# Performance work log

Measured on AMD Instinct MI355X. Metric: run time of the kernel, lower is better.

The kernel has to match this reference:

```python
import jax, jax.numpy as jnp
import numpy as np

N = 50000      # nodes
E = 800000     # edges (before self-loops)
F_IN = 128     # num_features
HID = 32       # hidden channels per head (conv1)
HEADS = 4      # conv1 heads
C = 40         # classes (conv2 out channels)
OUT_HEADS = 1  # conv2 heads
NEG_SLOPE = 0.2


def setup_inputs() -> dict:
    key = jax.random.key(0)
    ks = jax.random.split(key, 10)
    x = jax.random.normal(ks[0], (N, F_IN), jnp.float32)
    edge_index = jax.random.randint(ks[1], (2, E), 0, N, jnp.int32)
    s1 = 1.0 / np.sqrt(F_IN).astype(np.float32)
    s1h = 1.0 / np.sqrt(HID).astype(np.float32)
    s2 = 1.0 / np.sqrt(HEADS * HID).astype(np.float32)
    s2c = 1.0 / np.sqrt(C).astype(np.float32)
    W1 = jax.random.normal(ks[2], (F_IN, HEADS * HID), jnp.float32) * s1
    att_src1 = jax.random.normal(ks[3], (HEADS, HID), jnp.float32) * s1h
    att_dst1 = jax.random.normal(ks[4], (HEADS, HID), jnp.float32) * s1h
    bias1 = jnp.zeros((HEADS * HID,), jnp.float32)
    W2 = jax.random.normal(ks[5], (HEADS * HID, OUT_HEADS * C), jnp.float32) * s2
    att_src2 = jax.random.normal(ks[6], (OUT_HEADS, C), jnp.float32) * s2c
    att_dst2 = jax.random.normal(ks[7], (OUT_HEADS, C), jnp.float32) * s2c
    bias2 = jnp.zeros((C,), jnp.float32)
    return {"x": x, "edge_index": edge_index,
            "W1": W1, "att_src1": att_src1, "att_dst1": att_dst1, "bias1": bias1,
            "W2": W2, "att_src2": att_src2, "att_dst2": att_dst2, "bias2": bias2}


def gat_layer(h_in, src, dst, W, a_src, a_dst, bias, heads, out_ch, concat):
    """PyG GATConv (v1) in inference mode (no dropout on attention)."""
    n = h_in.shape[0]
    h = (h_in @ W).reshape(n, heads, out_ch)              # [N,H,F]
    e_src = jnp.einsum('nhf,hf->nh', h, a_src)            # [N,H]
    e_dst = jnp.einsum('nhf,hf->nh', h, a_dst)            # [N,H]
    alpha = jax.nn.leaky_relu(e_src[src] + e_dst[dst], NEG_SLOPE)  # [E,H]
    # segment softmax over destination-node neighborhoods
    amax = jax.ops.segment_max(alpha, dst, num_segments=n)
    amax = jnp.where(jnp.isfinite(amax), amax, 0.0)
    ex = jnp.exp(alpha - amax[dst])
    denom = jax.ops.segment_sum(ex, dst, num_segments=n)
    coef = ex / (denom[dst] + 1e-16)                      # [E,H]
    # scatter-aggregate weighted source messages
    out = jax.ops.segment_sum(h[src] * coef[:, :, None], dst, num_segments=n)  # [N,H,F]
    out = out.reshape(n, heads * out_ch) if concat else out.mean(axis=1)
    return out + bias


def reference(x, edge_index, W1, att_src1, att_dst1, bias1, W2, att_src2, att_dst2, bias2):
    n = x.shape[0]
    loop = jnp.arange(n, dtype=edge_index.dtype)          # GATConv adds self-loops
    src = jnp.concatenate([edge_index[0], loop])
    dst = jnp.concatenate([edge_index[1], loop])
    h = jax.nn.elu(gat_layer(x, src, dst, W1, att_src1, att_dst1, bias1, HEADS, HID, True))
    out = gat_layer(h, src, dst, W2, att_src2, att_dst2, bias2, OUT_HEADS, C, False)
    return (jax.nn.log_softmax(out, axis=1), jax.nn.softmax(out, axis=1))
```

## Files before the change

kernel.cpp:

```cpp
#include <hip/hip_runtime.h>
#include <hip/hip_bf16.h>

#define F1   128
#define H1   4
#define C2   40
#define NEG  0.2f
#define DS   96
#define EPB  1600
#define BCAP 5632

typedef __hip_bfloat16 bf16;
typedef float f32x2 __attribute__((ext_vector_type(2)));
typedef short s16x8 __attribute__((ext_vector_type(8)));
typedef float f32x4 __attribute__((ext_vector_type(4)));

__device__ __forceinline__ float ldf(const void* p, size_t i, int isbf) {
    return isbf ? __bfloat162float(((const bf16*)p)[i]) : ((const float*)p)[i];
}
__device__ __forceinline__ float lrelu(float a) { return a > 0.f ? a : NEG * a; }

__device__ __forceinline__ unsigned short f2bfb(float f, float& back) {
    unsigned u = __float_as_uint(f);
    unsigned r = u + 0x7FFFu + ((u >> 16) & 1u);
    unsigned short h = (unsigned short)(r >> 16);
    back = __uint_as_float((unsigned)h << 16);
    return h;
}

__device__ __forceinline__ void up2(unsigned g, float& lo, float& hi) {
    lo = __uint_as_float(g << 16);
    hi = __uint_as_float(g & 0xffff0000u);
}
__device__ __forceinline__ f32x2 up2v(unsigned g) {
    f32x2 r;
    r.x = __uint_as_float(g << 16);
    r.y = __uint_as_float(g & 0xffff0000u);
    return r;
}

__device__ __forceinline__ int excl_scan256(int v, int t, int* wsum) {
    int lane = t & 63, wid = t >> 6;
    int orig = v;
#pragma unroll
    for (int o = 1; o < 64; o <<= 1) {
        int n = __shfl_up(v, o, 64);
        if (lane >= o) v += n;
    }
    if (lane == 63) wsum[wid] = v;
    __syncthreads();
    int add = 0;
    for (int k = 0; k < wid; k++) add += wsum[k];
    return v + add - orig;
}

__global__ void k_prep(const unsigned short* __restrict__ x, const void* __restrict__ W1,
                       int* __restrict__ gbin_cnt, int* __restrict__ flag,
                       unsigned short* __restrict__ w1t_hi,
                       unsigned short* __restrict__ w1t_lo) {
    int t = threadIdx.x;
    __shared__ int sh[256];
    int cnt = 0;
    for (int k = t; k < 8192; k += 256)
        if (((x[k] >> 7) & 0xFF) >= 160) cnt++;
    sh[t] = cnt;
    __syncthreads();
    for (int s = 128; s > 0; s >>= 1) {
        if (t < s) sh[t] += sh[t + s];
        __syncthreads();
    }
    const int isbf = (sh[0] < 100) ? 1 : 0;
    if (blockIdx.x == 0) {
        gbin_cnt[t] = 0;
        if (t == 0) flag[0] = isbf;
    }
    int idx = blockIdx.x * 256 + t;
    int k = idx >> 7, c = idx & 127;
    float v = ldf(W1, idx, isbf);
    float back;
    unsigned short hi = f2bfb(v, back);
    float d2;
    unsigned short lo = f2bfb(v - back, d2);
    w1t_hi[c * 128 + k] = hi;
    w1t_lo[c * 128 + k] = isbf ? (unsigned short)0 : lo;
}

__global__ void __launch_bounds__(256) k_scatA(
        const int* __restrict__ ei, int E, int ET, int nbins,
        int* __restrict__ gbin_cnt, unsigned long long* __restrict__ stg) {
    __shared__ int hist[256], lstart[256], gbase[256], lcnt[256];
    __shared__ int wsum[4];
    __shared__ unsigned long long stgl[EPB];
    int t = threadIdx.x;
    hist[t] = 0; lcnt[t] = 0;
    __syncthreads();
    int e0 = blockIdx.x * EPB;
    int e1 = e0 + EPB; if (e1 > ET) e1 = ET;
    for (int e = e0 + t; e < e1; e += 256) {
        int d = (e < E) ? ei[E + e] : (e - E);
        atomicAdd(&hist[d >> 8], 1);
    }
    __syncthreads();
    if (t < nbins && hist[t] > 0) gbase[t] = atomicAdd(&gbin_cnt[t], hist[t]);
    int ls = excl_scan256(hist[t], t, wsum);
    lstart[t] = ls;
    __syncthreads();
    for (int e = e0 + t; e < e1; e += 256) {
        int s, d;
        if (e < E) { s = ei[e]; d = ei[E + e]; }
        else       { s = e - E; d = e - E; }
        int b = d >> 8;
        int r = atomicAdd(&lcnt[b], 1);
        stgl[lstart[b] + r] = ((unsigned long long)(unsigned)d << 32) | (unsigned)s;
    }
    __syncthreads();
    int cntb = e1 - e0;
    for (int i = t; i < cntb; i += 256) {
        unsigned long long p = stgl[i];
        int d = (int)(p >> 32);
        int b = d >> 8;
        int off = gbase[b] + (i - lstart[b]);
        if (off < BCAP) stg[(size_t)b * BCAP + off] = p;
    }
}

__global__ void __launch_bounds__(256) k_gemm1(
        const void* __restrict__ x, const unsigned short* __restrict__ w1t_hi,
        const unsigned short* __restrict__ w1t_lo,
        const void* __restrict__ as1, const void* __restrict__ ad1,
        const int* __restrict__ flag,
        const unsigned long long* __restrict__ stg, const int* __restrict__ gbin_cnt,
        int nbins, int* __restrict__ csr_s, int* __restrict__ rowstart,
        int* __restrict__ deg,
        bf16* __restrict__ h1b, float* __restrict__ es1, float* __restrict__ ed1,
        int N) {
    if (blockIdx.x < nbins) {
        __shared__ int dhist[256], dstart[256], dcnt[256];
        __shared__ int wsum[4];
        __shared__ int out_s[BCAP];
        int bin = blockIdx.x, tt = threadIdx.x;
        int bcnt = gbin_cnt[bin]; if (bcnt > BCAP) bcnt = BCAP;
        dhist[tt] = 0; dcnt[tt] = 0;
        __syncthreads();
        const unsigned long long* mystg = stg + (size_t)bin * BCAP;
        for (int i = tt; i < bcnt; i += 256)
            atomicAdd(&dhist[(int)(mystg[i] >> 32) & 255], 1);
        __syncthreads();
        int dsx = excl_scan256(dhist[tt], tt, wsum);
        dstart[tt] = dsx;
        __syncthreads();
        for (int i = tt; i < bcnt; i += 256) {
            unsigned long long p = mystg[i];
            int ld = (int)(p >> 32) & 255;
            int r = atomicAdd(&dcnt[ld], 1);
            out_s[dstart[ld] + r] = (int)(p & 0xffffffffu);
        }
        __syncthreads();
        size_t gb = (size_t)bin * BCAP;
        for (int i = tt; i < bcnt; i += 256) csr_s[gb + i] = out_s[i];
        int dd = bin * 256 + tt;
        if (dd < N) { rowstart[dd] = (int)gb + dstart[tt]; deg[dd] = dhist[tt]; }
        return;
    }
    const int isbf = flag[0];
    int t = threadIdx.x, wv = t >> 6, l = t & 63;
    int r0 = (wv & 1) * 16, c0 = (wv >> 1) * 64;
    int lr = l & 15, q = l >> 4;
    int n0 = (blockIdx.x - nbins) * 32;
    int rowa = n0 + r0 + lr; if (rowa >= N) rowa = N - 1;

    const bf16*  xb = (const bf16*)x;
    const float* xf = (const float*)x;
    f32x4 acc[4] = {};

#pragma unroll
    for (int ks = 0; ks < 4; ks++) {
        int kb = ks * 32 + q * 8;
        s16x8 ahi, alo;
        if (isbf) {
            ahi = *(const s16x8*)&xb[(size_t)rowa * 128 + kb];
        } else {
            const float* xr = xf + (size_t)rowa * 128 + kb;
            float4 v0 = *(const float4*)xr;
            float4 v1 = *(const float4*)(xr + 4);
            float vv[8] = {v0.x, v0.y, v0.z, v0.w, v1.x, v1.y, v1.z, v1.w};
#pragma unroll
            for (int j = 0; j < 8; j++) {
                float back;
                unsigned short hb = f2bfb(vv[j], back);
                float d2;
                unsigned short lb = f2bfb(vv[j] - back, d2);
                ahi[j] = (short)hb;
                alo[j] = (short)lb;
            }
        }
#pragma unroll
        for (int f = 0; f < 4; f++) {
            int col = c0 + f * 16 + lr;
            s16x8 bh = *(const s16x8*)&w1t_hi[(size_t)col * 128 + kb];
            acc[f] = __builtin_amdgcn_mfma_f32_16x16x32_bf16(ahi, bh, acc[f], 0, 0, 0);
            if (!isbf) {
                s16x8 bl = *(const s16x8*)&w1t_lo[(size_t)col * 128 + kb];
                acc[f] = __builtin_amdgcn_mfma_f32_16x16x32_bf16(alo, bh, acc[f], 0, 0, 0);
                acc[f] = __builtin_amdgcn_mfma_f32_16x16x32_bf16(ahi, bl, acc[f], 0, 0, 0);
            }
        }
    }

    float asv[4], adv[4];
#pragma unroll
    for (int f = 0; f < 4; f++) {
        asv[f] = ldf(as1, c0 + f * 16 + lr, isbf);
        adv[f] = ldf(ad1, c0 + f * 16 + lr, isbf);
    }
    float ps0[4], ps1[4], pd0[4], pd1[4];
#pragma unroll
    for (int r = 0; r < 4; r++) {
        int rw = n0 + r0 + q * 4 + r;
        ps0[r] = acc[0][r] * asv[0] + acc[1][r] * asv[1];
        ps1[r] = acc[2][r] * asv[2] + acc[3][r] * asv[3];
        pd0[r] = acc[0][r] * adv[0] + acc[1][r] * adv[1];
        pd1[r] = acc[2][r] * adv[2] + acc[3][r] * adv[3];
        if (rw < N) {
#pragma unroll
            for (int f = 0; f < 4; f++)
                h1b[(size_t)rw * 128 + c0 + f * 16 + lr] = __float2bfloat16(acc[f][r]);
        }
    }
#pragma unroll
    for (int off = 1; off < 16; off <<= 1) {
#pragma unroll
        for (int r = 0; r < 4; r++) {
            ps0[r] += __shfl_xor(ps0[r], off, 64);
            ps1[r] += __shfl_xor(ps1[r], off, 64);
            pd0[r] += __shfl_xor(pd0[r], off, 64);
            pd1[r] += __shfl_xor(pd1[r], off, 64);
        }
    }
    if (lr == 0) {
        int h0 = c0 >> 5;
#pragma unroll
        for (int r = 0; r < 4; r++) {
            int rw = n0 + r0 + q * 4 + r;
            if (rw < N) {
                es1[rw * H1 + h0]     = ps0[r];
                es1[rw * H1 + h0 + 1] = ps1[r];
                ed1[rw * H1 + h0]     = pd0[r];
                ed1[rw * H1 + h0 + 1] = pd1[r];
            }
        }
    }
}

__global__ void __launch_bounds__(256) k_l1(
        const int* __restrict__ deg, const int* __restrict__ rowstart,
        const int* __restrict__ csr_s,
        const float* __restrict__ es1, const float* __restrict__ ed1,
        const uint4* __restrict__ h1p4, const void* __restrict__ b1,
        const void* __restrict__ W2, const void* __restrict__ as2,
        const void* __restrict__ ad2, const int* __restrict__ flag,
        bf16* __restrict__ h2b, float* __restrict__ es2, float* __restrict__ ed2,
        int N) {
    int w = threadIdx.x >> 6, l = threadIdx.x & 63;
    int d = blockIdx.x * 4 + w; if (d >= N) d = N - 1;
    int cnt = deg[d]; if (cnt > DS) cnt = DS;
    int start = rowstart[d];

    __shared__ int   s_sh[4][DS];
    __shared__ float ev_sh[4][4][DS + 4];
    __shared__ float hs[4][144];

    float4 edv = *(const float4*)&ed1[(size_t)d * 4];
    float t0 = 0.f, t1 = 0.f, t2 = 0.f, t3 = 0.f;
    if (l < cnt) {
        int s = csr_s[start + l];
        s_sh[w][l] = s;
        float4 es4 = *(const float4*)&es1[(size_t)s * 4];
        float v0 = __expf(lrelu(es4.x + edv.x));
        float v1 = __expf(lrelu(es4.y + edv.y));
        float v2 = __expf(lrelu(es4.z + edv.z));
        float v3 = __expf(lrelu(es4.w + edv.w));
        ev_sh[w][0][l] = v0; ev_sh[w][1][l] = v1;
        ev_sh[w][2][l] = v2; ev_sh[w][3][l] = v3;
        t0 = v0; t1 = v1; t2 = v2; t3 = v3;
    }
    if (cnt > 64) {
        int l2 = 64 + l;
        if (l2 < cnt) {
            int s = csr_s[start + l2];
            s_sh[w][l2] = s;
            float4 es4 = *(const float4*)&es1[(size_t)s * 4];
            float v0 = __expf(lrelu(es4.x + edv.x));
            float v1 = __expf(lrelu(es4.y + edv.y));
            float v2 = __expf(lrelu(es4.z + edv.z));
            float v3 = __expf(lrelu(es4.w + edv.w));
            ev_sh[w][0][l2] = v0; ev_sh[w][1][l2] = v1;
            ev_sh[w][2][l2] = v2; ev_sh[w][3][l2] = v3;
            t0 += v0; t1 += v1; t2 += v2; t3 += v3;
        }
    }
#pragma unroll
    for (int o = 32; o > 0; o >>= 1) {
        t0 += __shfl_xor(t0, o, 64);
        t1 += __shfl_xor(t1, o, 64);
        t2 += __shfl_xor(t2, o, 64);
        t3 += __shfl_xor(t3, o, 64);
    }
    __syncthreads();

    int q = l >> 4, c16 = l & 15, h = c16 >> 2;
    f32x2 acc[4] = {{0.f, 0.f}, {0.f, 0.f}, {0.f, 0.f}, {0.f, 0.f}};
    for (int i = 0; i < cnt; i += 16) {
#pragma unroll
        for (int u = 0; u < 4; u++) {
            int e = i + q + 4 * u;
            int ec = min(e, cnt - 1);
            float evh = (e < cnt) ? ev_sh[w][h][ec] : 0.f;
            int s = s_sh[w][ec];
            uint4 g = h1p4[(size_t)s * 16 + c16];
            f32x2 ev2 = {evh, evh};
            acc[0] += ev2 * up2v(g.x);
            acc[1] += ev2 * up2v(g.y);
            acc[2] += ev2 * up2v(g.z);
            acc[3] += ev2 * up2v(g.w);
        }
    }

#pragma unroll
    for (int o = 16; o <= 32; o <<= 1) {
#pragma unroll
        for (int jj = 0; jj < 4; jj++) {
            acc[jj].x += __shfl_xor(acc[jj].x, o, 64);
            acc[jj].y += __shfl_xor(acc[jj].y, o, 64);
        }
    }

    const int isbf = flag[0];
    float dsum = (h == 0) ? t0 : (h == 1) ? t1 : (h == 2) ? t2 : t3;
    if (q == 0) {
        float inv = 1.f / (dsum + 1e-16f);
#pragma unroll
        for (int j = 0; j < 8; j++) {
            int col = c16 * 8 + j;
            float av = (j & 1) ? acc[j >> 1].y : acc[j >> 1].x;
            float v = av * inv + ldf(b1, col, isbf);
            hs[w][col + (col >> 3)] = v > 0.f ? v : (__expf(v) - 1.f);
        }
    }
    __syncthreads();
    float a2 = 0.f;
    if (l < C2) {
        if (isbf) {
            const bf16* W = (const bf16*)W2;
#pragma unroll 8
            for (int k = 0; k < F1; k++)
                a2 = fmaf(hs[w][k + (k >> 3)], __bfloat162float(W[(size_t)k * C2 + l]), a2);
        } else {
            const float* W = (const float*)W2;
#pragma unroll 8
            for (int k = 0; k < F1; k++)
                a2 = fmaf(hs[w][k + (k >> 3)], W[(size_t)k * C2 + l], a2);
        }
        h2b[(size_t)d * C2 + l] = __float2bfloat16(a2);
    }
    float ps = (l < C2) ? a2 * ldf(as2, l, isbf) : 0.f;
    float pd = (l < C2) ? a2 * ldf(ad2, l, isbf) : 0.f;
#pragma unroll
    for (int o = 32; o > 0; o >>= 1) {
        ps += __shfl_xor(ps, o, 64);
        pd += __shfl_xor(pd, o, 64);
    }
    if (l == 0) { es2[d] = ps; ed2[d] = pd; }
}

__global__ void __launch_bounds__(256) k_l2(
        const int* __restrict__ deg, const int* __restrict__ rowstart,
        const int* __restrict__ csr_s,
        const float* __restrict__ es2, const float* __restrict__ ed2,
        const uint2* __restrict__ h2p2, const void* __restrict__ b2,
        const int* __restrict__ flag, void* __restrict__ out, int N) {
    int w = threadIdx.x >> 6, l = threadIdx.x & 63;
    int d = blockIdx.x * 4 + w; if (d >= N) d = N - 1;
    int cnt = deg[d]; if (cnt > DS) cnt = DS;
    int start = rowstart[d];
    float edd = ed2[d];

    __shared__ int   s_sh2[4][DS];
    __shared__ float x_sh[4][DS];

    float xv = 0.f;
    if (l < cnt) {
        int s = csr_s[start + l];
        s_sh2[w][l] = s;
        xv = __expf(lrelu(es2[s] + edd));
        x_sh[w][l] = xv;
    }
    float dsum = xv;
    if (cnt > 64) {
        int l2 = 64 + l;
        if (l2 < cnt) {
            int s = csr_s[start + l2];
            s_sh2[w][l2] = s;
            float x2 = __expf(lrelu(es2[s] + edd));
            x_sh[w][l2] = x2;
            dsum += x2;
        }
    }
#pragma unroll
    for (int o = 32; o > 0; o >>= 1) dsum += __shfl_xor(dsum, o, 64);
    __syncthreads();

    int q = l >> 4, c10 = l & 15;
    bool act = c10 < 10;
    f32x2 acc0 = {0.f, 0.f}, acc1 = {0.f, 0.f};
    for (int i = 0; i < cnt; i += 16) {
#pragma unroll
        for (int u = 0; u < 4; u++) {
            int e = i + q + 4 * u;
            int ec = min(e, cnt - 1);
            float xc = (e < cnt) ? x_sh[w][ec] : 0.f;
            int s = s_sh2[w][ec];
            if (act) {
                uint2 g = h2p2[(size_t)s * 10 + c10];
                f32x2 x2 = {xc, xc};
                acc0 += x2 * up2v(g.x);
                acc1 += x2 * up2v(g.y);
            }
        }
    }
#pragma unroll
    for (int o = 16; o <= 32; o <<= 1) {
        acc0.x += __shfl_xor(acc0.x, o, 64); acc0.y += __shfl_xor(acc0.y, o, 64);
        acc1.x += __shfl_xor(acc1.x, o, 64); acc1.y += __shfl_xor(acc1.y, o, 64);
    }

    const int isbf = flag[0];
    float inv = 1.f / (dsum + 1e-16f);
    float v0 = -1e30f, v1 = -1e30f, v2 = -1e30f, v3 = -1e30f;
    if (act) {
        v0 = acc0.x * inv + ldf(b2, 4 * c10 + 0, isbf);
        v1 = acc0.y * inv + ldf(b2, 4 * c10 + 1, isbf);
        v2 = acc1.x * inv + ldf(b2, 4 * c10 + 2, isbf);
        v3 = acc1.y * inv + ldf(b2, 4 * c10 + 3, isbf);
    }
    float m = fmaxf(fmaxf(v0, v1), fmaxf(v2, v3));
#pragma unroll
    for (int o = 8; o > 0; o >>= 1) m = fmaxf(m, __shfl_xor(m, o, 16));
    float sv = act ? __expf(v0 - m) + __expf(v1 - m) + __expf(v2 - m) + __expf(v3 - m)
                   : 0.f;
#pragma unroll
    for (int o = 8; o > 0; o >>= 1) sv += __shfl_xor(sv, o, 16);
    float lse = m + __logf(sv);
    if (act && q == 0) {
        float ls0 = v0 - lse, ls1 = v1 - lse, ls2 = v2 - lse, ls3 = v3 - lse;
        size_t base = (size_t)d * C2 + 4 * c10, halfo = (size_t)N * C2;
        if (isbf) {
            bf16* o2 = (bf16*)out;
            o2[base + 0] = __float2bfloat16(ls0);
            o2[base + 1] = __float2bfloat16(ls1);
            o2[base + 2] = __float2bfloat16(ls2);
            o2[base + 3] = __float2bfloat16(ls3);
            o2[halfo + base + 0] = __float2bfloat16(__expf(ls0));
            o2[halfo + base + 1] = __float2bfloat16(__expf(ls1));
            o2[halfo + base + 2] = __float2bfloat16(__expf(ls2));
            o2[halfo + base + 3] = __float2bfloat16(__expf(ls3));
        } else {
            float4 lsv = {ls0, ls1, ls2, ls3};
            *(float4*)((float*)out + base) = lsv;
            float4 pv = {__expf(ls0), __expf(ls1), __expf(ls2), __expf(ls3)};
            *(float4*)((float*)out + halfo + base) = pv;
        }
    }
}

extern "C" void kernel_launch(void* const* d_in, const int* in_sizes, int n_in,
                              void* d_out, int out_size, void* d_ws, size_t ws_size,
                              hipStream_t stream) {
    const int N  = in_sizes[0] / F1;
    const int E  = in_sizes[1] / 2;
    const int ET = E + N;
    const int NBINS = (N + 255) >> 8;
    const int NBG = (N + 31) / 32;

    const void* x   = d_in[0];
    const int*  ei  = (const int*)d_in[1];
    const void* W1  = d_in[2];
    const void* as1 = d_in[3];
    const void* ad1 = d_in[4];
    const void* b1  = d_in[5];
    const void* W2  = d_in[6];
    const void* as2 = d_in[7];
    const void* ad2 = d_in[8];
    const void* b2  = d_in[9];

    float* ws = (float*)d_ws;
    auto al4 = [](size_t v) { return (v + 3) & ~(size_t)3; };
    size_t o = 0;
    bf16*  h1b  = (bf16*)(ws + o); o = al4(o + (size_t)64 * N);
    float* es1  = ws + o; o = al4(o + (size_t)H1 * N);
    float* ed1  = ws + o; o = al4(o + (size_t)H1 * N);
    bf16*  h2b  = (bf16*)(ws + o); o = al4(o + (size_t)20 * N);
    float* es2  = ws + o; o = al4(o + N);
    float* ed2  = ws + o; o = al4(o + N);
    int*   deg  = (int*)(ws + o); o = al4(o + N);
    int*   rowstart = (int*)(ws + o); o = al4(o + N);
    int*   gbin_cnt = (int*)(ws + o); o = al4(o + 256);
    int*   flag = (int*)(ws + o); o = al4(o + 4);
    int*   csr_s = (int*)(ws + o); o = al4(o + (size_t)NBINS * BCAP);
    unsigned short* w1t_hi = (unsigned short*)(ws + o); o = al4(o + 8192);
    unsigned short* w1t_lo = (unsigned short*)(ws + o); o = al4(o + 8192);
    unsigned long long* stg = (unsigned long long*)(ws + o);
    o = al4(o + (size_t)2 * NBINS * BCAP);

    k_prep<<<64, 256, 0, stream>>>((const unsigned short*)x, W1, gbin_cnt, flag,
                                   w1t_hi, w1t_lo);
    k_scatA<<<(ET + EPB - 1) / EPB, 256, 0, stream>>>(ei, E, ET, NBINS, gbin_cnt, stg);
    k_gemm1<<<NBINS + NBG, 256, 0, stream>>>(x, w1t_hi, w1t_lo, as1, ad1, flag,
                                             stg, gbin_cnt, NBINS, csr_s, rowstart,
                                             deg, h1b, es1, ed1, N);
    k_l1<<<(N + 3) / 4, 256, 0, stream>>>(deg, rowstart, csr_s, es1, ed1,
                                          (const uint4*)h1b, b1, W2, as2, ad2, flag,
                                          h2b, es2, ed2, N);
    k_l2<<<(N + 3) / 4, 256, 0, stream>>>(deg, rowstart, csr_s, es2, ed2,
                                          (const uint2*)h2b, b2, flag, d_out, N);
}
```

Measured before the change: 281.8 us.

## Merge prep and edge-scatter kernels; pad h2 rows for 16-byte gathers

The W1 prep work and the edge binning scatter now run as one launch, split by block index, and gbin_cnt is zeroed with a memset instead of inside the prep kernel. This removes one kernel launch and lets the two independent jobs overlap. Layer-2 features are stored with a 64-element row stride (128-byte aligned), so k_l2 gathers with uint4 loads across 5 lanes per edge instead of uint2 across 10. The padding uses more workspace and leaves more lanes idle per gather, in exchange for fewer and wider memory transactions.

```diff
diff --git a/kernel.cpp b/kernel.cpp
--- a/kernel.cpp
+++ b/kernel.cpp
@@ -53,47 +53,44 @@
     return v + add - orig;
 }
 
-__global__ void k_prep(const unsigned short* __restrict__ x, const void* __restrict__ W1,
-                       int* __restrict__ gbin_cnt, int* __restrict__ flag,
-                       unsigned short* __restrict__ w1t_hi,
-                       unsigned short* __restrict__ w1t_lo) {
+__global__ void __launch_bounds__(256) k_prepA(
+        const unsigned short* __restrict__ x, const void* __restrict__ W1,
+        const int* __restrict__ ei, int E, int ET, int nbins,
+        int* __restrict__ gbin_cnt, int* __restrict__ flag,
+        unsigned short* __restrict__ w1t_hi, unsigned short* __restrict__ w1t_lo,
+        unsigned long long* __restrict__ stg) {
     int t = threadIdx.x;
-    __shared__ int sh[256];
-    int cnt = 0;
-    for (int k = t; k < 8192; k += 256)
-        if (((x[k] >> 7) & 0xFF) >= 160) cnt++;
-    sh[t] = cnt;
-    __syncthreads();
-    for (int s = 128; s > 0; s >>= 1) {
-        if (t < s) sh[t] += sh[t + s];
+    if (blockIdx.x < 64) {
+        __shared__ int sh[256];
+        int cnt = 0;
+        for (int k = t; k < 8192; k += 256)
+            if (((x[k] >> 7) & 0xFF) >= 160) cnt++;
+        sh[t] = cnt;
         __syncthreads();
-    }
-    const int isbf = (sh[0] < 100) ? 1 : 0;
-    if (blockIdx.x == 0) {
-        gbin_cnt[t] = 0;
-        if (t == 0) flag[0] = isbf;
-    }
-    int idx = blockIdx.x * 256 + t;
-    int k = idx >> 7, c = idx & 127;
-    float v = ldf(W1, idx, isbf);
-    float back;
-    unsigned short hi = f2bfb(v, back);
-    float d2;
-    unsigned short lo = f2bfb(v - back, d2);
-    w1t_hi[c * 128 + k] = hi;
-    w1t_lo[c * 128 + k] = isbf ? (unsigned short)0 : lo;
-}
-
-__global__ void __launch_bounds__(256) k_scatA(
-        const int* __restrict__ ei, int E, int ET, int nbins,
-        int* __restrict__ gbin_cnt, unsigned long long* __restrict__ stg) {
+        for (int s = 128; s > 0; s >>= 1) {
+            if (t < s) sh[t] += sh[t + s];
+            __syncthreads();
+        }
+        const int isbf = (sh[0] < 100) ? 1 : 0;
+        if (blockIdx.x == 0 && t == 0) flag[0] = isbf;
+        int idx = blockIdx.x * 256 + t;
+        int k = idx >> 7, c = idx & 127;
+        float v = ldf(W1, idx, isbf);
+        float back;
+        unsigned short hi = f2bfb(v, back);
+        float d2;
+        unsigned short lo = f2bfb(v - back, d2);
+        w1t_hi[c * 128 + k] = hi;
+        w1t_lo[c * 128 + k] = isbf ? (unsigned short)0 : lo;
+        return;
+    }
     __shared__ int hist[256], lstart[256], gbase[256], lcnt[256];
     __shared__ int wsum[4];
     __shared__ unsigned long long stgl[EPB];
-    int t = threadIdx.x;
     hist[t] = 0; lcnt[t] = 0;
     __syncthreads();
-    int e0 = blockIdx.x * EPB;
+    int bs = blockIdx.x - 64;
+    int e0 = bs * EPB;
     int e1 = e0 + EPB; if (e1 > ET) e1 = ET;
     for (int e = e0 + t; e < e1; e += 256) {
         int d = (e < E) ? ei[E + e] : (e - E);
@@ -360,7 +357,7 @@
             for (int k = 0; k < F1; k++)
                 a2 = fmaf(hs[w][k + (k >> 3)], W[(size_t)k * C2 + l], a2);
         }
-        h2b[(size_t)d * C2 + l] = __float2bfloat16(a2);
+        h2b[(size_t)d * 64 + l] = __float2bfloat16(a2);
     }
     float ps = (l < C2) ? a2 * ldf(as2, l, isbf) : 0.f;
     float pd = (l < C2) ? a2 * ldf(ad2, l, isbf) : 0.f;
@@ -376,7 +373,7 @@
         const int* __restrict__ deg, const int* __restrict__ rowstart,
         const int* __restrict__ csr_s,
         const float* __restrict__ es2, const float* __restrict__ ed2,
-        const uint2* __restrict__ h2p2, const void* __restrict__ b2,
+        const uint4* __restrict__ h2p4, const void* __restrict__ b2,
         const int* __restrict__ flag, void* __restrict__ out, int N) {
     int w = threadIdx.x >> 6, l = threadIdx.x & 63;
     int d = blockIdx.x * 4 + w; if (d >= N) d = N - 1;
@@ -409,9 +406,9 @@
     for (int o = 32; o > 0; o >>= 1) dsum += __shfl_xor(dsum, o, 64);
     __syncthreads();
 
-    int q = l >> 4, c10 = l & 15;
-    bool act = c10 < 10;
-    f32x2 acc0 = {0.f, 0.f}, acc1 = {0.f, 0.f};
+    int q = l >> 4, c16 = l & 15;
+    bool act = c16 < 5;
+    f32x2 acc[4] = {{0.f, 0.f}, {0.f, 0.f}, {0.f, 0.f}, {0.f, 0.f}};
     for (int i = 0; i < cnt; i += 16) {
 #pragma unroll
         for (int u = 0; u < 4; u++) {
@@ -420,54 +417,70 @@
             float xc = (e < cnt) ? x_sh[w][ec] : 0.f;
             int s = s_sh2[w][ec];
             if (act) {
-                uint2 g = h2p2[(size_t)s * 10 + c10];
+                uint4 g = h2p4[(size_t)s * 8 + c16];
                 f32x2 x2 = {xc, xc};
-                acc0 += x2 * up2v(g.x);
-                acc1 += x2 * up2v(g.y);
+                acc[0] += x2 * up2v(g.x);
+                acc[1] += x2 * up2v(g.y);
+                acc[2] += x2 * up2v(g.z);
+                acc[3] += x2 * up2v(g.w);
             }
         }
     }
 #pragma unroll
     for (int o = 16; o <= 32; o <<= 1) {
-        acc0.x += __shfl_xor(acc0.x, o, 64); acc0.y += __shfl_xor(acc0.y, o, 64);
-        acc1.x += __shfl_xor(acc1.x, o, 64); acc1.y += __shfl_xor(acc1.y, o, 64);
+#pragma unroll
+        for (int jj = 0; jj < 4; jj++) {
+            acc[jj].x += __shfl_xor(acc[jj].x, o, 64);
+            acc[jj].y += __shfl_xor(acc[jj].y, o, 64);
+        }
     }
 
     const int isbf = flag[0];
     float inv = 1.f / (dsum + 1e-16f);
-    float v0 = -1e30f, v1 = -1e30f, v2 = -1e30f, v3 = -1e30f;
+    float v[8];
+#pragma unroll
+    for (int j = 0; j < 8; j++) v[j] = -1e30f;
     if (act) {
-        v0 = acc0.x * inv + ldf(b2, 4 * c10 + 0, isbf);
-        v1 = acc0.y * inv + ldf(b2, 4 * c10 + 1, isbf);
-        v2 = acc1.x * inv + ldf(b2, 4 * c10 + 2, isbf);
-        v3 = acc1.y * inv + ldf(b2, 4 * c10 + 3, isbf);
-    }
-    float m = fmaxf(fmaxf(v0, v1), fmaxf(v2, v3));
+#pragma unroll
+        for (int j = 0; j < 8; j++) {
+            float av = (j & 1) ? acc[j >> 1].y : acc[j >> 1].x;
+            v[j] = av * inv + ldf(b2, 8 * c16 + j, isbf);
+        }
+    }
+    float m = v[0];
+#pragma unroll
+    for (int j = 1; j < 8; j++) m = fmaxf(m, v[j]);
 #pragma unroll
     for (int o = 8; o > 0; o >>= 1) m = fmaxf(m, __shfl_xor(m, o, 16));
-    float sv = act ? __expf(v0 - m) + __expf(v1 - m) + __expf(v2 - m) + __expf(v3 - m)
-                   : 0.f;
+    float sv = 0.f;
+    if (act) {
+#pragma unroll
+        for (int j = 0; j < 8; j++) sv += __expf(v[j] - m);
+    }
 #pragma unroll
     for (int o = 8; o > 0; o >>= 1) sv += __shfl_xor(sv, o, 16);
     float lse = m + __logf(sv);
     if (act && q == 0) {
-        float ls0 = v0 - lse, ls1 = v1 - lse, ls2 = v2 - lse, ls3 = v3 - lse;
-        size_t base = (size_t)d * C2 + 4 * c10, halfo = (size_t)N * C2;
+        size_t base = (size_t)d * C2 + 8 * c16, halfo = (size_t)N * C2;
         if (isbf) {
             bf16* o2 = (bf16*)out;
-            o2[base + 0] = __float2bfloat16(ls0);
-            o2[base + 1] = __float2bfloat16(ls1);
-            o2[base + 2] = __float2bfloat16(ls2);
-            o2[base + 3] = __float2bfloat16(ls3);
-            o2[halfo + base + 0] = __float2bfloat16(__expf(ls0));
-            o2[halfo + base + 1] = __float2bfloat16(__expf(ls1));
-            o2[halfo + base + 2] = __float2bfloat16(__expf(ls2));
-            o2[halfo + base + 3] = __float2bfloat16(__expf(ls3));
+#pragma unroll
+            for (int j = 0; j < 8; j++) {
+                float lsj = v[j] - lse;
+                o2[base + j] = __float2bfloat16(lsj);
+                o2[halfo + base + j] = __float2bfloat16(__expf(lsj));
+            }
         } else {
-            float4 lsv = {ls0, ls1, ls2, ls3};
-            *(float4*)((float*)out + base) = lsv;
-            float4 pv = {__expf(ls0), __expf(ls1), __expf(ls2), __expf(ls3)};
-            *(float4*)((float*)out + halfo + base) = pv;
+            float* o2 = (float*)out;
+            float4 lo, hi, plo, phi;
+            lo.x = v[0] - lse; lo.y = v[1] - lse; lo.z = v[2] - lse; lo.w = v[3] - lse;
+            hi.x = v[4] - lse; hi.y = v[5] - lse; hi.z = v[6] - lse; hi.w = v[7] - lse;
+            plo.x = __expf(lo.x); plo.y = __expf(lo.y); plo.z = __expf(lo.z); plo.w = __expf(lo.w);
+            phi.x = __expf(hi.x); phi.y = __expf(hi.y); phi.z = __expf(hi.z); phi.w = __expf(hi.w);
+            *(float4*)(o2 + base) = lo;
+            *(float4*)(o2 + base + 4) = hi;
+            *(float4*)(o2 + halfo + base) = plo;
+            *(float4*)(o2 + halfo + base + 4) = phi;
         }
     }
 }
@@ -479,6 +492,7 @@
     const int E  = in_sizes[1] / 2;
     const int ET = E + N;
     const int NBINS = (N + 255) >> 8;
+    const int NSA = (ET + EPB - 1) / EPB;
     const int NBG = (N + 31) / 32;
 
     const void* x   = d_in[0];
@@ -493,12 +507,14 @@
     const void* b2  = d_in[9];
 
     float* ws = (float*)d_ws;
-    auto al4 = [](size_t v) { return (v + 3) & ~(size_t)3; };
+    auto al4  = [](size_t v) { return (v + 3) & ~(size_t)3; };
+    auto al32 = [](size_t v) { return (v + 31) & ~(size_t)31; };
     size_t o = 0;
     bf16*  h1b  = (bf16*)(ws + o); o = al4(o + (size_t)64 * N);
     float* es1  = ws + o; o = al4(o + (size_t)H1 * N);
     float* ed1  = ws + o; o = al4(o + (size_t)H1 * N);
-    bf16*  h2b  = (bf16*)(ws + o); o = al4(o + (size_t)20 * N);
+    o = al32(o);
+    bf16*  h2b  = (bf16*)(ws + o); o = al4(o + (size_t)32 * N);
     float* es2  = ws + o; o = al4(o + N);
     float* ed2  = ws + o; o = al4(o + N);
     int*   deg  = (int*)(ws + o); o = al4(o + N);
@@ -511,9 +527,9 @@
     unsigned long long* stg = (unsigned long long*)(ws + o);
     o = al4(o + (size_t)2 * NBINS * BCAP);
 
-    k_prep<<<64, 256, 0, stream>>>((const unsigned short*)x, W1, gbin_cnt, flag,
-                                   w1t_hi, w1t_lo);
-    k_scatA<<<(ET + EPB - 1) / EPB, 256, 0, stream>>>(ei, E, ET, NBINS, gbin_cnt, stg);
+    hipMemsetAsync(gbin_cnt, 0, 256 * sizeof(int), stream);
+    k_prepA<<<64 + NSA, 256, 0, stream>>>((const unsigned short*)x, W1, ei, E, ET,
+                                          NBINS, gbin_cnt, flag, w1t_hi, w1t_lo, stg);
     k_gemm1<<<NBINS + NBG, 256, 0, stream>>>(x, w1t_hi, w1t_lo, as1, ad1, flag,
                                              stg, gbin_cnt, NBINS, csr_s, rowstart,
                                              deg, h1b, es1, ed1, N);
@@ -521,5 +537,5 @@
                                           (const uint4*)h1b, b1, W2, as2, ad2, flag,
                                           h2b, es2, ed2, N);
     k_l2<<<(N + 3) / 4, 256, 0, stream>>>(deg, rowstart, csr_s, es2, ed2,
-                                          (const uint2*)h2b, b2, flag, d_out, N);
-}
+                                          (const uint4*)h2b, b2, flag, d_out, N);
+}
```

Result: no change. 279.7 us (median of 2 runs) (-0.7%).
